# Kernel tuning notes

Measured on AMD Instinct MI355X. Metric: run time of the kernel, lower is better.

Reference implementation:

```python
import jax, jax.numpy as jnp
import numpy as np

B, T, E, H = 4, 1024, 2048, 32
D = E // H
BITS = 8


def fake_quant(x, axis=-1, bits=BITS):
    # dynamic asymmetric fake quantization (find_params + quantize + dequantize)
    maxq = float(2 ** bits - 1)
    xmax = jnp.maximum(jnp.max(x, axis=axis, keepdims=True), 0.0)
    xmin = jnp.minimum(jnp.min(x, axis=axis, keepdims=True), 0.0)
    scale = (xmax - xmin) / maxq
    scale = jnp.where(scale <= 0.0, 1.0, scale)
    zero = jnp.round(-xmin / scale)
    q = jnp.clip(jnp.round(x / scale) + zero, 0.0, maxq)
    return scale * (q - zero)


def setup_inputs() -> dict:
    key = jax.random.key(0)
    ks = jax.random.split(key, 9)
    std = 0.02
    hidden_states = jax.random.normal(ks[0], (B, T, E), jnp.float32)
    wq = jax.random.normal(ks[1], (E, E), jnp.float32) * std
    wk = jax.random.normal(ks[2], (E, E), jnp.float32) * std
    wv = jax.random.normal(ks[3], (E, E), jnp.float32) * std
    wo = jax.random.normal(ks[4], (E, E), jnp.float32) * std
    bq = jax.random.normal(ks[5], (E,), jnp.float32) * std
    bk = jax.random.normal(ks[6], (E,), jnp.float32) * std
    bv = jax.random.normal(ks[7], (E,), jnp.float32) * std
    bo = jax.random.normal(ks[8], (E,), jnp.float32) * std
    causal = jnp.tril(jnp.ones((T, T), dtype=bool))
    attention_mask = jnp.where(causal, 0.0, -1e9).astype(jnp.float32)[None, None]  # [1,1,T,T]
    return dict(hidden_states=hidden_states, wq=wq, bq=bq, wk=wk, bk=bk,
                wv=wv, bv=bv, wo=wo, bo=bo, attention_mask=attention_mask)


def reference(hidden_states, wq, bq, wk, bk, wv, bv, wo, bo, attention_mask):
    b, t, e = hidden_states.shape
    h, d = H, e // H
    scaling = d ** -0.5

    def split_heads(x):
        return x.reshape(b, t, h, d).transpose(0, 2, 1, 3)  # [b,h,t,d]

    q = split_heads((hidden_states @ wq.T + bq) * scaling)
    k = split_heads(hidden_states @ wk.T + bk)
    v = split_heads(hidden_states @ wv.T + bv)

    # SmoothK per_channel: divide K by per-channel (over tokens) abs-max, quantize
    # in the smoothed domain, rescale back.
    s = jnp.clip(jnp.max(jnp.abs(k), axis=2, keepdims=True), 1e-5, None)  # [b,h,1,d]
    k = fake_quant(k / s, axis=-1) * s

    q = fake_quant(q, axis=-1)           # per-token quant of Q
    v = fake_quant(v, axis=2)            # V quantized along sequence (transpose(2,3) path)

    attn = jnp.einsum('bhqd,bhkd->bhqk', q, k) + attention_mask
    probs = jax.nn.softmax(attn.astype(jnp.float32), axis=-1).astype(q.dtype)
    # dropout p=0 (eval); attn-weight quantization happens after probs are taken,
    # so it does not affect attn_output.
    out = jnp.einsum('bhqk,bhkd->bhqd', probs, v)
    out = out.transpose(0, 2, 1, 3).reshape(b, t, e)
    return out @ wo.T + bo
```

## Files before the change

### kernel.cpp

```cpp
#include <hip/hip_runtime.h>
#include <hip/hip_bf16.h>

typedef __hip_bfloat16 bf16;
typedef __attribute__((ext_vector_type(4))) short short4v;
typedef __attribute__((ext_vector_type(8))) short short8;
typedef __attribute__((ext_vector_type(4))) float f32x4;

#define NB 4
#define NT 1024
#define NE 2048
#define NH 32
#define ND 64
#define NBH (NB*NH)

__device__ __forceinline__ short bf16bits(float x) {
    bf16 h = __float2bfloat16(x);
    return *reinterpret_cast<short*>(&h);
}
__device__ __forceinline__ float bitsbf16(short s) {
    bf16 h = *reinterpret_cast<bf16*>(&s);
    return __bfloat162float(h);
}

__device__ __forceinline__ void gll16(const bf16* g, bf16* l) {
    __builtin_amdgcn_global_load_lds(
        (const __attribute__((address_space(1))) unsigned int*)g,
        (__attribute__((address_space(3))) unsigned int*)l, 16, 0, 0);
}

__global__ void detect_dtype(const unsigned short* __restrict__ w, int* __restrict__ flag) {
    int l = threadIdx.x;
    int big = 0;
    for (int i = l; i < 512; i += 64) {
        unsigned e = (w[i] >> 7) & 0xFFu;
        if (e >= 0x88u) big = 1;
    }
    unsigned long long m = __ballot(big != 0);
    if (l == 0) *flag = (m != 0ULL) ? 1 : 0;
}

__global__ __launch_bounds__(256) void conv_all(
    const void* __restrict__ hs, const void* __restrict__ wq, const void* __restrict__ wk,
    const void* __restrict__ wv, const void* __restrict__ wo,
    bf16* __restrict__ dhs, bf16* __restrict__ dwq, bf16* __restrict__ dwk,
    bf16* __restrict__ dwv, bf16* __restrict__ dwo, const int* __restrict__ flagp)
{
    const bool f32 = (*flagp != 0);
    int bid = blockIdx.x;
    const void* src; bf16* dst; size_t blk;
    if (bid < 4096)      { src = hs; dst = dhs; blk = bid; }
    else {
        int r = (bid - 4096) >> 11, o = (bid - 4096) & 2047;
        blk = o;
        src = r == 0 ? wq : (r == 1 ? wk : (r == 2 ? wv : wo));
        dst = r == 0 ? dwq : (r == 1 ? dwk : (r == 2 ? dwv : dwo));
    }
    size_t i = (blk * 256 + threadIdx.x) * 8;
    if (f32) {
        const float* s = (const float*)src + i;
        f32x4 a = *(const f32x4*)s;
        f32x4 b = *(const f32x4*)(s + 4);
        short8 r8;
        r8[0] = bf16bits(a[0]); r8[1] = bf16bits(a[1]);
        r8[2] = bf16bits(a[2]); r8[3] = bf16bits(a[3]);
        r8[4] = bf16bits(b[0]); r8[5] = bf16bits(b[1]);
        r8[6] = bf16bits(b[2]); r8[7] = bf16bits(b[3]);
        *(short8*)(dst + i) = r8;
    } else {
        *(short8*)(dst + i) = *(const short8*)((const bf16*)src + i);
    }
}

__global__ __launch_bounds__(256) void gemm_qkv(
    const bf16* __restrict__ A,
    const bf16* __restrict__ Wq, const bf16* __restrict__ Wk, const bf16* __restrict__ Wv,
    const void* __restrict__ bq, const void* __restrict__ bk, const void* __restrict__ bv,
    bf16* __restrict__ Qb, bf16* __restrict__ Kb, bf16* __restrict__ Vt,
    const int* __restrict__ flagp,
    int* __restrict__ sKb, int* __restrict__ vMx, int* __restrict__ vNg)
{
    const int K = NE, z = blockIdx.z;
    const bf16* W = z == 0 ? Wq : (z == 1 ? Wk : Wv);
    const void* bias = z == 0 ? bq : (z == 1 ? bk : bv);
    const float scale = z == 0 ? 0.125f : 1.0f;

    __shared__ __align__(16) bf16 As[128 * 32];
    __shared__ __align__(16) bf16 Ws[128 * 32];
    int tid = threadIdx.x;
    int w = tid >> 6, l = tid & 63;
    int lr = l & 15, quad = l >> 4;
    int mBase = blockIdx.y * 128, nBase = blockIdx.x * 128;
    int mw = (w >> 1) * 64, nw = (w & 1) * 64;
    f32x4 acc[4][4] = {};

    const bf16* Ag = A + (size_t)(mBase + w * 16 + (l >> 2)) * K + (l & 3) * 8;
    const bf16* Wg = W + (size_t)(nBase + w * 16 + (l >> 2)) * K + (l & 3) * 8;
    bf16* AsW = As + (w * 16) * 32;
    bf16* WsW = Ws + (w * 16) * 32;

    for (int k0 = 0; k0 < K; k0 += 32) {
        gll16(Ag + k0, AsW);
        gll16(Ag + (size_t)64 * K + k0, AsW + 64 * 32);
        gll16(Wg + k0, WsW);
        gll16(Wg + (size_t)64 * K + k0, WsW + 64 * 32);
        __syncthreads();
        short8 af[4], bfr[4];
        #pragma unroll
        for (int i = 0; i < 4; i++)
            af[i] = *(const short8*)(As + (mw + i * 16 + lr) * 32 + quad * 8);
        #pragma unroll
        for (int j = 0; j < 4; j++)
            bfr[j] = *(const short8*)(Ws + (nw + j * 16 + lr) * 32 + quad * 8);
        #pragma unroll
        for (int i = 0; i < 4; i++)
            #pragma unroll
            for (int j = 0; j < 4; j++)
                acc[i][j] = __builtin_amdgcn_mfma_f32_16x16x32_bf16(
                    af[i], bfr[j], acc[i][j], 0, 0, 0);
        __syncthreads();
    }

    const bool f32 = (*flagp != 0);
    float bv4[4];
    #pragma unroll
    for (int j = 0; j < 4; j++) {
        int n = nBase + nw + j * 16 + lr;
        bv4[j] = f32 ? ((const float*)bias)[n] : bitsbf16(((const short*)bias)[n]);
    }
    float colA[4] = {0.f, 0.f, 0.f, 0.f};
    float colB[4] = {0.f, 0.f, 0.f, 0.f};

    #pragma unroll
    for (int i = 0; i < 4; i++) {
        float v[4][4];
        #pragma unroll
        for (int j = 0; j < 4; j++)
            #pragma unroll
            for (int r = 0; r < 4; r++)
                v[j][r] = (acc[i][j][r] + bv4[j]) * scale;

        if (z == 0) {
            #pragma unroll
            for (int r = 0; r < 4; r++) {
                float mx = 0.f, mn = 0.f;
                #pragma unroll
                for (int j = 0; j < 4; j++) { mx = fmaxf(mx, v[j][r]); mn = fminf(mn, v[j][r]); }
                #pragma unroll
                for (int off = 1; off < 16; off <<= 1) {
                    mx = fmaxf(mx, __shfl_xor(mx, off));
                    mn = fminf(mn, __shfl_xor(mn, off));
                }
                float sc = (mx - mn) * (1.f / 255.f);
                if (sc <= 0.f) sc = 1.f;
                float zq = rintf(-mn / sc);
                #pragma unroll
                for (int j = 0; j < 4; j++) {
                    float q = fminf(fmaxf(rintf(v[j][r] / sc) + zq, 0.f), 255.f);
                    v[j][r] = sc * (q - zq);
                }
            }
        } else if (z == 1) {
            #pragma unroll
            for (int j = 0; j < 4; j++)
                #pragma unroll
                for (int r = 0; r < 4; r++)
                    colA[j] = fmaxf(colA[j], fabsf(v[j][r]));
        } else {
            #pragma unroll
            for (int j = 0; j < 4; j++)
                #pragma unroll
                for (int r = 0; r < 4; r++) {
                    colA[j] = fmaxf(colA[j], v[j][r]);
                    colB[j] = fmaxf(colB[j], -v[j][r]);
                }
        }

        #pragma unroll
        for (int j = 0; j < 4; j++) {
            int n = nBase + nw + j * 16 + lr;
            int h = n >> 6, d = n & (ND - 1);
            #pragma unroll
            for (int r = 0; r < 4; r++) {
                int m = mBase + mw + i * 16 + quad * 4 + r;
                int b = m >> 10, t = m & (NT - 1);
                if (z == 0)
                    Qb[(((size_t)(b * NH + h)) * NT + t) * ND + d] = (bf16)v[j][r];
                else if (z == 1)
                    Kb[(((size_t)(b * NH + h)) * NT + t) * ND + d] = (bf16)v[j][r];
                else
                    Vt[(((size_t)(b * NH + h)) * ND + d) * NT + t] = (bf16)v[j][r];
            }
        }
    }

    if (z >= 1) {
        int b = mBase >> 10;
        #pragma unroll
        for (int j = 0; j < 4; j++) {
            float a = colA[j], c = colB[j];
            a = fmaxf(a, __shfl_xor(a, 16)); a = fmaxf(a, __shfl_xor(a, 32));
            if (z == 2) { c = fmaxf(c, __shfl_xor(c, 16)); c = fmaxf(c, __shfl_xor(c, 32)); }
            if (quad == 0) {
                int n = nBase + nw + j * 16 + lr;
                int idx = (b * NH + (n >> 6)) * 64 + (n & 63);
                if (z == 1) atomicMax(sKb + idx, __float_as_int(a));
                else { atomicMax(vMx + idx, __float_as_int(a)); atomicMax(vNg + idx, __float_as_int(c)); }
            }
        }
    }
}

__global__ __launch_bounds__(256) void gemm_o(
    const bf16* __restrict__ A, const bf16* __restrict__ W,
    const void* __restrict__ bias, void* __restrict__ out, const int* __restrict__ flagp)
{
    const int K = NE, N = NE;
    __shared__ __align__(16) bf16 As[128 * 32];
    __shared__ __align__(16) bf16 Ws[128 * 32];
    int tid = threadIdx.x;
    int w = tid >> 6, l = tid & 63;
    int lr = l & 15, quad = l >> 4;
    int mBase = blockIdx.y * 128, nBase = blockIdx.x * 128;
    int mw = (w >> 1) * 64, nw = (w & 1) * 64;
    f32x4 acc[4][4] = {};

    const bf16* Ag = A + (size_t)(mBase + w * 16 + (l >> 2)) * K + (l & 3) * 8;
    const bf16* Wg = W + (size_t)(nBase + w * 16 + (l >> 2)) * K + (l & 3) * 8;
    bf16* AsW = As + (w * 16) * 32;
    bf16* WsW = Ws + (w * 16) * 32;

    for (int k0 = 0; k0 < K; k0 += 32) {
        gll16(Ag + k0, AsW);
        gll16(Ag + (size_t)64 * K + k0, AsW + 64 * 32);
        gll16(Wg + k0, WsW);
        gll16(Wg + (size_t)64 * K + k0, WsW + 64 * 32);
        __syncthreads();
        short8 af[4], bfr[4];
        #pragma unroll
        for (int i = 0; i < 4; i++)
            af[i] = *(const short8*)(As + (mw + i * 16 + lr) * 32 + quad * 8);
        #pragma unroll
        for (int j = 0; j < 4; j++)
            bfr[j] = *(const short8*)(Ws + (nw + j * 16 + lr) * 32 + quad * 8);
        #pragma unroll
        for (int i = 0; i < 4; i++)
            #pragma unroll
            for (int j = 0; j < 4; j++)
                acc[i][j] = __builtin_amdgcn_mfma_f32_16x16x32_bf16(
                    af[i], bfr[j], acc[i][j], 0, 0, 0);
        __syncthreads();
    }

    const bool f32 = (*flagp != 0);
    #pragma unroll
    for (int i = 0; i < 4; i++) {
        #pragma unroll
        for (int j = 0; j < 4; j++) {
            int n = nBase + nw + j * 16 + lr;
            float bv = f32 ? ((const float*)bias)[n] : bitsbf16(((const short*)bias)[n]);
            #pragma unroll
            for (int r = 0; r < 4; r++) {
                int m = mBase + mw + i * 16 + quad * 4 + r;
                float vv = acc[i][j][r] + bv;
                if (f32) ((float*)out)[(size_t)m * N + n] = vv;
                else     ((bf16*)out)[(size_t)m * N + n] = (bf16)vv;
            }
        }
    }
}

__global__ __launch_bounds__(256) void quant_kv(
    bf16* __restrict__ Kb, bf16* __restrict__ Vt,
    const int* __restrict__ sKbits, const int* __restrict__ vMax, const int* __restrict__ vNeg)
{
    int bh = blockIdx.y;
    if (blockIdx.x < 256) {
        int t = blockIdx.x * 4 + (threadIdx.x >> 6);
        int l = threadIdx.x & 63;
        size_t idx = ((size_t)bh * NT + t) * ND + l;
        float s = fmaxf(__int_as_float(sKbits[bh * 64 + l]), 1e-5f);
        float x = (float)Kb[idx] / s;
        float mx = fmaxf(x, 0.f), mn = fminf(x, 0.f);
        #pragma unroll
        for (int off = 1; off < 64; off <<= 1) {
            mx = fmaxf(mx, __shfl_xor(mx, off));
            mn = fminf(mn, __shfl_xor(mn, off));
        }
        float sc = (mx - mn) * (1.f / 255.f);
        if (sc <= 0.f) sc = 1.f;
        float z = rintf(-mn / sc);
        float q = fminf(fmaxf(rintf(x / sc) + z, 0.f), 255.f);
        Kb[idx] = (bf16)(s * (sc * (q - z)));
    } else {
        int d = (blockIdx.x - 256) * 8 + (threadIdx.x >> 5);
        int c = (threadIdx.x & 31) * 8;
        float mx = __int_as_float(vMax[bh * 64 + d]);
        float mn = -__int_as_float(vNeg[bh * 64 + d]);
        float sc = (mx - mn) * (1.f / 255.f);
        if (sc <= 0.f) sc = 1.f;
        float z = rintf(-mn / sc);
        bf16* row = Vt + ((size_t)bh * ND + d) * NT;
        for (int seg = 0; seg < 4; seg++) {
            int off = seg * 256 + c;
            short8 v8 = *(const short8*)(row + off);
            #pragma unroll
            for (int k = 0; k < 8; k++) {
                float f = bitsbf16(v8[k]);
                float q = fminf(fmaxf(rintf(f / sc) + z, 0.f), 255.f);
                v8[k] = bf16bits(sc * (q - z));
            }
            *(short8*)(row + off) = v8;
        }
    }
}

__global__ __launch_bounds__(256) void attn3(
    const bf16* __restrict__ Q, const bf16* __restrict__ K,
    const bf16* __restrict__ Vt, bf16* __restrict__ O)
{
    int bh = blockIdx.y;
    int b = bh >> 5, h = bh & 31;
    int qb = (int)gridDim.x - 1 - (int)blockIdx.x;
    int qBase = qb * 64;
    int w = threadIdx.x >> 6, l = threadIdx.x & 63;
    int lr = l & 15, quad = l >> 4;
    int qRow = qBase + w * 16;

    __shared__ __align__(16) bf16 Ks[2][64 * 64];
    __shared__ __align__(16) bf16 Vs[2][64 * 64];
    __shared__ __align__(16) bf16 Psh[4][16 * 64];

    const bf16* Kbase = K + (size_t)bh * NT * ND;
    const bf16* Vbase = Vt + (size_t)bh * ND * NT;

    const bf16* Qp = Q + ((size_t)bh * NT + qRow + lr) * ND + quad * 8;
    short8 qf0 = *(const short8*)Qp;
    short8 qf1 = *(const short8*)(Qp + 32);

    f32x4 o[4] = {};
    float m_i[4], l_i[4];
    #pragma unroll
    for (int r = 0; r < 4; r++) { m_i[r] = -1e30f; l_i[r] = 0.f; }

    int nkt = qb + 1;
    int srow = w * 16 + (l >> 3);
    int scol = (((l & 7) ^ ((l >> 3) & 7))) * 8;

    auto stage = [&](int kt, int bufi) {
        int kc0 = kt * 64;
        #pragma unroll
        for (int c = 0; c < 2; c++) {
            gll16(Kbase + (size_t)(kc0 + srow + c * 8) * ND + scol,
                  &Ks[bufi][(w * 16 + c * 8) * 64]);
            gll16(Vbase + (size_t)(srow + c * 8) * NT + kc0 + scol,
                  &Vs[bufi][(w * 16 + c * 8) * 64]);
        }
    };
    stage(0, 0);

    int slot0 = (quad ^ (lr & 7)) * 8;
    int slot1 = ((quad ^ 4) ^ (lr & 7)) * 8;

    for (int kt = 0; kt < nkt; kt++) {
        __syncthreads();
        if (kt + 1 < nkt) stage(kt + 1, (kt + 1) & 1);
        const bf16* Kt = Ks[kt & 1];
        const bf16* Vv = Vs[kt & 1];
        int kc0 = kt * 64;

        f32x4 s[4] = {};
        #pragma unroll
        for (int nb = 0; nb < 4; nb++) {
            short8 b0 = *(const short8*)(Kt + (nb * 16 + lr) * 64 + slot0);
            short8 b1 = *(const short8*)(Kt + (nb * 16 + lr) * 64 + slot1);
            s[nb] = __builtin_amdgcn_mfma_f32_16x16x32_bf16(qf0, b0, s[nb], 0, 0, 0);
            s[nb] = __builtin_amdgcn_mfma_f32_16x16x32_bf16(qf1, b1, s[nb], 0, 0, 0);
        }

        int row0 = qRow + quad * 4;
        float rmax[4];
        #pragma unroll
        for (int r = 0; r < 4; r++) rmax[r] = -1e30f;
        if (kt == qb) {
            #pragma unroll
            for (int nb = 0; nb < 4; nb++) {
                int col = kc0 + nb * 16 + lr;
                #pragma unroll
                for (int r = 0; r < 4; r++) {
                    if (col > row0 + r) s[nb][r] = -1e30f;
                    rmax[r] = fmaxf(rmax[r], s[nb][r]);
                }
            }
        } else {
            #pragma unroll
            for (int nb = 0; nb < 4; nb++)
                #pragma unroll
                for (int r = 0; r < 4; r++)
                    rmax[r] = fmaxf(rmax[r], s[nb][r]);
        }
        #pragma unroll
        for (int off = 1; off < 16; off <<= 1)
            #pragma unroll
            for (int r = 0; r < 4; r++)
                rmax[r] = fmaxf(rmax[r], __shfl_xor(rmax[r], off));

        float alpha[4], rsum[4];
        #pragma unroll
        for (int r = 0; r < 4; r++) {
            float mn2 = fmaxf(m_i[r], rmax[r]);
            alpha[r] = __expf(m_i[r] - mn2);
            m_i[r] = mn2;
            rsum[r] = 0.f;
        }
        #pragma unroll
        for (int nb = 0; nb < 4; nb++) {
            int cb = nb * 2 + (lr >> 3), ci = lr & 7;
            #pragma unroll
            for (int r = 0; r < 4; r++) {
                float pp = __expf(s[nb][r] - m_i[r]);
                rsum[r] += pp;
                int row = quad * 4 + r;
                Psh[w][row * 64 + (cb ^ (row & 7)) * 8 + ci] = (bf16)pp;
            }
        }
        #pragma unroll
        for (int off = 1; off < 16; off <<= 1)
            #pragma unroll
            for (int r = 0; r < 4; r++)
                rsum[r] += __shfl_xor(rsum[r], off);
        #pragma unroll
        for (int r = 0; r < 4; r++) l_i[r] = l_i[r] * alpha[r] + rsum[r];
        #pragma unroll
        for (int f = 0; f < 4; f++)
            #pragma unroll
            for (int r = 0; r < 4; r++)
                o[f][r] *= alpha[r];

        __syncthreads();
        short8 p0 = *(const short8*)(&Psh[w][lr * 64 + slot0]);
        short8 p1 = *(const short8*)(&Psh[w][lr * 64 + slot1]);
        #pragma unroll
        for (int f = 0; f < 4; f++) {
            short8 v0 = *(const short8*)(Vv + (f * 16 + lr) * 64 + slot0);
            short8 v1 = *(const short8*)(Vv + (f * 16 + lr) * 64 + slot1);
            o[f] = __builtin_amdgcn_mfma_f32_16x16x32_bf16(p0, v0, o[f], 0, 0, 0);
            o[f] = __builtin_amdgcn_mfma_f32_16x16x32_bf16(p1, v1, o[f], 0, 0, 0);
        }
    }

    float inv[4];
    #pragma unroll
    for (int r = 0; r < 4; r++) inv[r] = 1.f / l_i[r];
    #pragma unroll
    for (int f = 0; f < 4; f++)
        #pragma unroll
        for (int r = 0; r < 4; r++) {
            int t = qRow + quad * 4 + r;
            int d = f * 16 + lr;
            O[((size_t)(b * NT + t)) * NE + h * ND + d] = (bf16)(o[f][r] * inv[r]);
        }
}

__device__ __forceinline__ void stage_tile(const void* __restrict__ src, bool f32,
                                           int rowBase, int k0, bf16* dst, int tid)
{
    const int K = NE;
    if (f32) {
        int r = tid >> 3;
        int c = (tid & 7) * 4;
        const float* p = (const float*)src + (size_t)(rowBase + r) * K + k0 + c;
        bf16* d = dst + r * 32 + c;
        #pragma unroll
        for (int i = 0; i < 4; i++) {
            f32x4 v = *(const f32x4*)(p + (size_t)(i * 32) * K);
            short4v o;
            o[0] = bf16bits(v[0]); o[1] = bf16bits(v[1]);
            o[2] = bf16bits(v[2]); o[3] = bf16bits(v[3]);
            *(short4v*)(d + i * 32 * 32) = o;
        }
    } else {
        int r = tid >> 2;
        int c = (tid & 3) * 8;
        const bf16* p = (const bf16*)src + (size_t)(rowBase + r) * K + k0 + c;
        bf16* d = dst + r * 32 + c;
        #pragma unroll
        for (int i = 0; i < 2; i++)
            *(short8*)(d + i * 64 * 32) = *(const short8*)(p + (size_t)(i * 64) * K);
    }
}

template<bool A_DYN, int MODE>
__global__ __launch_bounds__(256) void gemm_bt(
    const void* __restrict__ A, const void* __restrict__ W,
    const void* __restrict__ bias, float scale, void* __restrict__ out,
    const int* __restrict__ flagp)
{
    const int K = NE, N = NE;
    const bool f32 = (*flagp != 0);
    __shared__ __align__(16) bf16 As[128 * 32];
    __shared__ __align__(16) bf16 Ws[128 * 32];
    int tid = threadIdx.x;
    int w = tid >> 6, l = tid & 63;
    int lr = l & 15, quad = l >> 4;
    int mBase = blockIdx.y * 128;
    int nBase = blockIdx.x * 128;
    int mw = (w >> 1) * 64, nw = (w & 1) * 64;
    f32x4 acc[4][4] = {};
    for (int k0 = 0; k0 < K; k0 += 32) {
        stage_tile(A, A_DYN && f32, mBase, k0, As, tid);
        stage_tile(W, f32, nBase, k0, Ws, tid);
        __syncthreads();
        short8 af[4], bfr[4];
        #pragma unroll
        for (int i = 0; i < 4; i++)
            af[i] = *(const short8*)(As + (mw + i * 16 + lr) * 32 + quad * 8);
        #pragma unroll
        for (int j = 0; j < 4; j++)
            bfr[j] = *(const short8*)(Ws + (nw + j * 16 + lr) * 32 + quad * 8);
        #pragma unroll
        for (int i = 0; i < 4; i++)
            #pragma unroll
            for (int j = 0; j < 4; j++)
                acc[i][j] = __builtin_amdgcn_mfma_f32_16x16x32_bf16(
                    af[i], bfr[j], acc[i][j], 0, 0, 0);
        __syncthreads();
    }
    #pragma unroll
    for (int i = 0; i < 4; i++) {
        #pragma unroll
        for (int j = 0; j < 4; j++) {
            int n = nBase + nw + j * 16 + lr;
            float bv = f32 ? ((const float*)bias)[n] : bitsbf16(((const short*)bias)[n]);
            #pragma unroll
            for (int r = 0; r < 4; r++) {
                int m = mBase + mw + i * 16 + quad * 4 + r;
                float v = (acc[i][j][r] + bv) * scale;
                if (MODE == 0) {
                    if (f32) ((float*)out)[(size_t)m * N + n] = v;
                    else     ((bf16*)out)[(size_t)m * N + n] = (bf16)v;
                } else {
                    int b = m >> 10, t = m & (NT - 1);
                    int h = n >> 6, d = n & (ND - 1);
                    if (MODE == 1)
                        ((bf16*)out)[(((size_t)(b * NH + h)) * NT + t) * ND + d] = (bf16)v;
                    else
                        ((bf16*)out)[(((size_t)(b * NH + h)) * ND + d) * NT + t] = (bf16)v;
                }
            }
        }
    }
}

__global__ __launch_bounds__(256) void stats_k(
    const bf16* __restrict__ K, float* __restrict__ sK)
{
    int bh = blockIdx.x;
    int d = threadIdx.x & 63, tg = threadIdx.x >> 6;
    const bf16* Kp = K + (size_t)bh * NT * ND;
    float kabs = 0.f;
    for (int t = tg; t < NT; t += 4)
        kabs = fmaxf(kabs, fabsf((float)Kp[t * ND + d]));
    __shared__ float sh[4][64];
    sh[tg][d] = kabs;
    __syncthreads();
    if (threadIdx.x < 64) {
        kabs = fmaxf(fmaxf(sh[0][d], sh[1][d]), fmaxf(sh[2][d], sh[3][d]));
        sK[bh * 64 + d] = fmaxf(kabs, 1e-5f);
    }
}

__global__ __launch_bounds__(256) void stats_v(
    const bf16* __restrict__ Vt, float* __restrict__ vScale, float* __restrict__ vZero)
{
    int bh = blockIdx.x;
    int c = threadIdx.x >> 2;
    int seg = threadIdx.x & 3;
    const bf16* row = Vt + ((size_t)bh * ND + c) * NT + seg * 256;
    float vmax = 0.f, vmin = 0.f;
    for (int i = 0; i < 256; i += 8) {
        short8 v8 = *(const short8*)(row + i);
        for (int j = 0; j < 8; j++) {
            float f = bitsbf16(v8[j]);
            vmax = fmaxf(vmax, f);
            vmin = fminf(vmin, f);
        }
    }
    vmax = fmaxf(vmax, __shfl_xor(vmax, 1));
    vmax = fmaxf(vmax, __shfl_xor(vmax, 2));
    vmin = fminf(vmin, __shfl_xor(vmin, 1));
    vmin = fminf(vmin, __shfl_xor(vmin, 2));
    if (seg == 0) {
        float sc = (vmax - vmin) * (1.f / 255.f);
        if (sc <= 0.f) sc = 1.f;
        vScale[bh * 64 + c] = sc;
        vZero[bh * 64 + c] = rintf(-vmin / sc);
    }
}

__global__ __launch_bounds__(256) void quant_qk(
    bf16* __restrict__ Q, bf16* __restrict__ K, const float* __restrict__ sK)
{
    int bh = blockIdx.y;
    int t = blockIdx.x * 4 + (threadIdx.x >> 6);
    int l = threadIdx.x & 63;
    size_t idx = ((size_t)bh * NT + t) * ND + l;
    {
        float x = (float)Q[idx];
        float xmax = fmaxf(x, 0.f), xmin = fminf(x, 0.f);
        for (int off = 1; off < 64; off <<= 1) {
            xmax = fmaxf(xmax, __shfl_xor(xmax, off));
            xmin = fminf(xmin, __shfl_xor(xmin, off));
        }
        float sc = (xmax - xmin) * (1.f / 255.f);
        if (sc <= 0.f) sc = 1.f;
        float z = rintf(-xmin / sc);
        float q = fminf(fmaxf(rintf(x / sc) + z, 0.f), 255.f);
        Q[idx] = (bf16)(sc * (q - z));
    }
    {
        float s = sK[bh * 64 + l];
        float x = (float)K[idx] / s;
        float xmax = fmaxf(x, 0.f), xmin = fminf(x, 0.f);
        for (int off = 1; off < 64; off <<= 1) {
            xmax = fmaxf(xmax, __shfl_xor(xmax, off));
            xmin = fminf(xmin, __shfl_xor(xmin, off));
        }
        float sc = (xmax - xmin) * (1.f / 255.f);
        if (sc <= 0.f) sc = 1.f;
        float z = rintf(-xmin / sc);
        float q = fminf(fmaxf(rintf(x / sc) + z, 0.f), 255.f);
        K[idx] = (bf16)(s * (sc * (q - z)));
    }
}

__global__ __launch_bounds__(256) void quant_v_old(
    bf16* __restrict__ Vt,
    const float* __restrict__ vScale, const float* __restrict__ vZero)
{
    int bh = blockIdx.y, d = blockIdx.x;
    float sc = vScale[bh * 64 + d], z = vZero[bh * 64 + d];
    bf16* row = Vt + ((size_t)bh * ND + d) * NT;
    for (int t = threadIdx.x; t < NT; t += 256) {
        float v = (float)row[t];
        float q = fminf(fmaxf(rintf(v / sc) + z, 0.f), 255.f);
        row[t] = (bf16)(sc * (q - z));
    }
}

extern "C" void kernel_launch(void* const* d_in, const int* in_sizes, int n_in,
                              void* d_out, int out_size, void* d_ws, size_t ws_size,
                              hipStream_t stream)
{
    (void)in_sizes; (void)n_in; (void)out_size;
    const void* hs = d_in[0];
    const void* wq = d_in[1];
    const void* bq = d_in[2];
    const void* wk = d_in[3];
    const void* bk = d_in[4];
    const void* wv = d_in[5];
    const void* bv = d_in[6];
    const void* wo = d_in[7];
    const void* bo = d_in[8];

    const size_t qkvE = (size_t)NBH * NT * ND;
    const size_t qkvB = qkvE * 2;
    const size_t wBy  = (size_t)NE * NE * 2;
    const size_t statB = 3 * (size_t)NBH * ND * 4;
    const size_t needFast = 4 * qkvB + 4 * wBy + statB + 256;

    dim3 blk(256);
    dim3 gG(NE / 128, (NB * NT) / 128);
    const float scaling = 0.125f;

    if (ws_size >= needFast) {
        char* p = (char*)d_ws;
        bf16* Qb  = (bf16*)p; p += qkvB;
        bf16* Kb  = (bf16*)p; p += qkvB;
        bf16* Vt  = (bf16*)p; p += qkvB;
        bf16* hsB = (bf16*)p; p += qkvB;
        bf16* wqB = (bf16*)p; p += wBy;
        bf16* wkB = (bf16*)p; p += wBy;
        bf16* wvB = (bf16*)p; p += wBy;
        bf16* woB = (bf16*)p; p += wBy;
        int* sKb = (int*)p;
        int* vMx = sKb + NBH * ND;
        int* vNg = vMx + NBH * ND;
        int* flag = vNg + NBH * ND;
        bf16* Ab = hsB;

        detect_dtype<<<dim3(1), dim3(64), 0, stream>>>((const unsigned short*)wq, flag);
        hipMemsetAsync(sKb, 0, statB, stream);
        conv_all<<<dim3(4096 + 4 * 2048), blk, 0, stream>>>(
            hs, wq, wk, wv, wo, hsB, wqB, wkB, wvB, woB, flag);
        gemm_qkv<<<dim3(NE / 128, (NB * NT) / 128, 3), blk, 0, stream>>>(
            hsB, wqB, wkB, wvB, bq, bk, bv, Qb, Kb, Vt, flag, sKb, vMx, vNg);
        quant_kv<<<dim3(256 + ND / 8, NBH), blk, 0, stream>>>(Kb, Vt, sKb, vMx, vNg);
        attn3<<<dim3(NT / 64, NBH), blk, 0, stream>>>(Qb, Kb, Vt, Ab);
        gemm_o<<<gG, blk, 0, stream>>>(Ab, woB, bo, d_out, flag);
    } else {
        bf16* Qb = (bf16*)d_ws;
        bf16* Kb = Qb + qkvE;
        bf16* Vt = Kb + qkvE;
        bf16* Ab = Vt + qkvE;
        float* sK  = (float*)(Ab + qkvE);
        float* vSc = sK + NBH * ND;
        float* vZp = vSc + NBH * ND;
        int*   flag = (int*)(vZp + NBH * ND);

        detect_dtype<<<dim3(1), dim3(64), 0, stream>>>((const unsigned short*)wq, flag);
        gemm_bt<true, 1><<<gG, blk, 0, stream>>>(hs, wq, bq, scaling, Qb, flag);
        gemm_bt<true, 1><<<gG, blk, 0, stream>>>(hs, wk, bk, 1.0f, Kb, flag);
        gemm_bt<true, 2><<<gG, blk, 0, stream>>>(hs, wv, bv, 1.0f, Vt, flag);
        stats_k<<<dim3(NBH), blk, 0, stream>>>(Kb, sK);
        stats_v<<<dim3(NBH), blk, 0, stream>>>(Vt, vSc, vZp);
        quant_qk<<<dim3(NT / 4, NBH), blk, 0, stream>>>(Qb, Kb, sK);
        quant_v_old<<<dim3(ND, NBH), blk, 0, stream>>>(Vt, vSc, vZp);
        attn3<<<dim3(NT / 64, NBH), blk, 0, stream>>>(Qb, Kb, Vt, Ab);
        gemm_bt<false, 0><<<gG, blk, 0, stream>>>(Ab, wo, bo, 1.0f, d_out, flag);
    }
}
```

Before: 503.2 us.

## Load GEMM weight fragments directly to registers with K=64 tiles and XOR-swizzled LDS

Both the QKV and output projection GEMMs stop staging the weight tile in shared memory. Each wave now reads its B fragments straight from global memory into registers, while the A tile is staged alone in LDS at a K-step of 64 with an XOR swizzle to avoid bank conflicts. This halves the number of loop iterations and barriers and cuts LDS traffic. In exchange, weight loads become uncoalesced per-lane 16-byte reads that are repeated by the two waves sharing the same columns, and register pressure goes up.

```diff
diff --git a/kernel.cpp b/kernel.cpp
--- a/kernel.cpp
+++ b/kernel.cpp
@@ -84,8 +84,7 @@
     const void* bias = z == 0 ? bq : (z == 1 ? bk : bv);
     const float scale = z == 0 ? 0.125f : 1.0f;
 
-    __shared__ __align__(16) bf16 As[128 * 32];
-    __shared__ __align__(16) bf16 Ws[128 * 32];
+    __shared__ __align__(16) bf16 As[128 * 64];
     int tid = threadIdx.x;
     int w = tid >> 6, l = tid & 63;
     int lr = l & 15, quad = l >> 4;
@@ -93,30 +92,36 @@
     int mw = (w >> 1) * 64, nw = (w & 1) * 64;
     f32x4 acc[4][4] = {};
 
-    const bf16* Ag = A + (size_t)(mBase + w * 16 + (l >> 2)) * K + (l & 3) * 8;
-    const bf16* Wg = W + (size_t)(nBase + w * 16 + (l >> 2)) * K + (l & 3) * 8;
-    bf16* AsW = As + (w * 16) * 32;
-    bf16* WsW = Ws + (w * 16) * 32;
-
-    for (int k0 = 0; k0 < K; k0 += 32) {
-        gll16(Ag + k0, AsW);
-        gll16(Ag + (size_t)64 * K + k0, AsW + 64 * 32);
-        gll16(Wg + k0, WsW);
-        gll16(Wg + (size_t)64 * K + k0, WsW + 64 * 32);
+    int srow = w * 32 + (l >> 3);
+    int scol = ((l & 7) ^ ((l >> 3) & 7)) * 8;
+    const bf16* Ag = A + (size_t)(mBase + srow) * K + scol;
+    bf16* AsW = As + (w * 32) * 64;
+
+    const bf16* Wp = W + (size_t)(nBase + nw + lr) * K + quad * 8;
+
+    for (int k0 = 0; k0 < K; k0 += 64) {
+        #pragma unroll
+        for (int c = 0; c < 4; c++)
+            gll16(Ag + (size_t)(c * 8) * K + k0, AsW + (c * 8) * 64);
+        short8 bfr[4][2];
+        #pragma unroll
+        for (int j = 0; j < 4; j++)
+            #pragma unroll
+            for (int h = 0; h < 2; h++)
+                bfr[j][h] = *(const short8*)(Wp + (size_t)(j * 16) * K + k0 + h * 32);
         __syncthreads();
-        short8 af[4], bfr[4];
-        #pragma unroll
-        for (int i = 0; i < 4; i++)
-            af[i] = *(const short8*)(As + (mw + i * 16 + lr) * 32 + quad * 8);
-        #pragma unroll
-        for (int j = 0; j < 4; j++)
-            bfr[j] = *(const short8*)(Ws + (nw + j * 16 + lr) * 32 + quad * 8);
-        #pragma unroll
-        for (int i = 0; i < 4; i++)
-            #pragma unroll
-            for (int j = 0; j < 4; j++)
-                acc[i][j] = __builtin_amdgcn_mfma_f32_16x16x32_bf16(
-                    af[i], bfr[j], acc[i][j], 0, 0, 0);
+        #pragma unroll
+        for (int i = 0; i < 4; i++) {
+            #pragma unroll
+            for (int h = 0; h < 2; h++) {
+                short8 a8 = *(const short8*)(
+                    As + (mw + i * 16 + lr) * 64 + (((h * 4 + quad) ^ (lr & 7)) * 8));
+                #pragma unroll
+                for (int j = 0; j < 4; j++)
+                    acc[i][j] = __builtin_amdgcn_mfma_f32_16x16x32_bf16(
+                        a8, bfr[j][h], acc[i][j], 0, 0, 0);
+            }
+        }
         __syncthreads();
     }
 
@@ -215,8 +220,7 @@
     const void* __restrict__ bias, void* __restrict__ out, const int* __restrict__ flagp)
 {
     const int K = NE, N = NE;
-    __shared__ __align__(16) bf16 As[128 * 32];
-    __shared__ __align__(16) bf16 Ws[128 * 32];
+    __shared__ __align__(16) bf16 As[128 * 64];
     int tid = threadIdx.x;
     int w = tid >> 6, l = tid & 63;
     int lr = l & 15, quad = l >> 4;
@@ -224,30 +228,35 @@
     int mw = (w >> 1) * 64, nw = (w & 1) * 64;
     f32x4 acc[4][4] = {};
 
-    const bf16* Ag = A + (size_t)(mBase + w * 16 + (l >> 2)) * K + (l & 3) * 8;
-    const bf16* Wg = W + (size_t)(nBase + w * 16 + (l >> 2)) * K + (l & 3) * 8;
-    bf16* AsW = As + (w * 16) * 32;
-    bf16* WsW = Ws + (w * 16) * 32;
-
-    for (int k0 = 0; k0 < K; k0 += 32) {
-        gll16(Ag + k0, AsW);
-        gll16(Ag + (size_t)64 * K + k0, AsW + 64 * 32);
-        gll16(Wg + k0, WsW);
-        gll16(Wg + (size_t)64 * K + k0, WsW + 64 * 32);
+    int srow = w * 32 + (l >> 3);
+    int scol = ((l & 7) ^ ((l >> 3) & 7)) * 8;
+    const bf16* Ag = A + (size_t)(mBase + srow) * K + scol;
+    bf16* AsW = As + (w * 32) * 64;
+    const bf16* Wp = W + (size_t)(nBase + nw + lr) * K + quad * 8;
+
+    for (int k0 = 0; k0 < K; k0 += 64) {
+        #pragma unroll
+        for (int c = 0; c < 4; c++)
+            gll16(Ag + (size_t)(c * 8) * K + k0, AsW + (c * 8) * 64);
+        short8 bfr[4][2];
+        #pragma unroll
+        for (int j = 0; j < 4; j++)
+            #pragma unroll
+            for (int h = 0; h < 2; h++)
+                bfr[j][h] = *(const short8*)(Wp + (size_t)(j * 16) * K + k0 + h * 32);
         __syncthreads();
-        short8 af[4], bfr[4];
-        #pragma unroll
-        for (int i = 0; i < 4; i++)
-            af[i] = *(const short8*)(As + (mw + i * 16 + lr) * 32 + quad * 8);
-        #pragma unroll
-        for (int j = 0; j < 4; j++)
-            bfr[j] = *(const short8*)(Ws + (nw + j * 16 + lr) * 32 + quad * 8);
-        #pragma unroll
-        for (int i = 0; i < 4; i++)
-            #pragma unroll
-            for (int j = 0; j < 4; j++)
-                acc[i][j] = __builtin_amdgcn_mfma_f32_16x16x32_bf16(
-                    af[i], bfr[j], acc[i][j], 0, 0, 0);
+        #pragma unroll
+        for (int i = 0; i < 4; i++) {
+            #pragma unroll
+            for (int h = 0; h < 2; h++) {
+                short8 a8 = *(const short8*)(
+                    As + (mw + i * 16 + lr) * 64 + (((h * 4 + quad) ^ (lr & 7)) * 8));
+                #pragma unroll
+                for (int j = 0; j < 4; j++)
+                    acc[i][j] = __builtin_amdgcn_mfma_f32_16x16x32_bf16(
+                        a8, bfr[j][h], acc[i][j], 0, 0, 0);
+            }
+        }
         __syncthreads();
     }
 
```

Result: slower. 602.1 us (+19.6%).
